# Kernel tuning notes

Measured on AMD Instinct MI355X. Metric: run time of the kernel, lower is better.

Reference implementation:

```python
import jax, jax.numpy as jnp
import numpy as np

B, T1, T2, D, M = 64, 128, 160, 768, 64


def setup_inputs() -> dict:
    key = jax.random.key(0)
    k1, k2, k3 = jax.random.split(key, 3)
    v1 = jax.random.normal(k1, (B, T1, D), dtype=jnp.float32)
    v2 = jax.random.normal(k2, (B, T2, D), dtype=jnp.float32)
    # keras 'uniform' initializer: U(-0.05, 0.05); kernel logical shape (1,1,M,D) -> (M,D)
    kernel = jax.random.uniform(k3, (M, D), dtype=jnp.float32, minval=-0.05, maxval=0.05)
    return {"v1": v1, "v2": v2, "kernel": kernel}


def reference(v1, v2, kernel):
    # Original: expand v1 to [b,t1,1,m,d]*kernel, v2 to [b,1,t2,1,d],
    # numerator = sum_d(v1*v2), cosine_norm=False -> tanh(numerator).
    # Fused as a single einsum contraction over d (avoids [b,t1,t2,m,d] intermediate).
    num = jnp.einsum('bid,md,bjd->bijm', v1, kernel, v2)  # [b,t1,t2,m]
    return jnp.tanh(num)
```

## Files before the change

### kernel.cpp

```cpp
#include <hip/hip_runtime.h>
#include <hip/hip_bf16.h>

namespace {

constexpr int Bn = 64, T1 = 128, T2 = 160, D = 768, M = 64;
constexpr int NTOT = T2 * M;
constexpr int BM = 128;
constexpr int BN = 128;
constexpr int BK = 32;
constexpr int KSTEPS = D / BK;

typedef __bf16 bf16x8 __attribute__((ext_vector_type(8)));
typedef __bf16 bf16x4 __attribute__((ext_vector_type(4)));
typedef float  f32x4  __attribute__((ext_vector_type(4)));

__device__ __forceinline__ float fast_tanh(float x) {
  float e = __expf(2.0f * x);
  return 1.0f - 2.0f * __builtin_amdgcn_rcpf(e + 1.0f);
}

__global__ void cvt_bf16(const float* __restrict__ x, __bf16* __restrict__ y, int n4) {
  int i = blockIdx.x * blockDim.x + threadIdx.x;
  if (i < n4) {
    f32x4 v = ((const f32x4*)x)[i];
    bf16x4 o;
    o[0] = (__bf16)v.x; o[1] = (__bf16)v.y; o[2] = (__bf16)v.z; o[3] = (__bf16)v.w;
    ((bf16x4*)y)[i] = o;
  }
}

__device__ __forceinline__ bf16x8 mul_bb(uint4 a, uint4 b) {
  const unsigned hm = 0xffff0000u;
  bf16x8 r;
  float al, ah, bl, bh;
  al = __uint_as_float(a.x << 16); ah = __uint_as_float(a.x & hm);
  bl = __uint_as_float(b.x << 16); bh = __uint_as_float(b.x & hm);
  r[0] = (__bf16)(al * bl); r[1] = (__bf16)(ah * bh);
  al = __uint_as_float(a.y << 16); ah = __uint_as_float(a.y & hm);
  bl = __uint_as_float(b.y << 16); bh = __uint_as_float(b.y & hm);
  r[2] = (__bf16)(al * bl); r[3] = (__bf16)(ah * bh);
  al = __uint_as_float(a.z << 16); ah = __uint_as_float(a.z & hm);
  bl = __uint_as_float(b.z << 16); bh = __uint_as_float(b.z & hm);
  r[4] = (__bf16)(al * bl); r[5] = (__bf16)(ah * bh);
  al = __uint_as_float(a.w << 16); ah = __uint_as_float(a.w & hm);
  bl = __uint_as_float(b.w << 16); bh = __uint_as_float(b.w & hm);
  r[6] = (__bf16)(al * bl); r[7] = (__bf16)(ah * bh);
  return r;
}

__launch_bounds__(256, 4)
__global__ void mpcos_fast(const __bf16* __restrict__ v1b,
                           const __bf16* __restrict__ v2b,
                           const __bf16* __restrict__ kb,
                           float* __restrict__ out) {
  __shared__ __bf16 Al[2][BM * BK];
  __shared__ __bf16 Bl[2][BN * BK];

  const int t    = threadIdx.x;
  const int lane = t & 63;
  const int w    = t >> 6;
  const int bjm  = blockIdx.x;
  const int bb   = blockIdx.y;

  const int sm = t >> 2, sc = t & 3;
  const __bf16* kp   = kb + sm * D + sc * 8;
  const __bf16* v2p0 = v2b + ((size_t)(bb * T2 + bjm * 2)) * D + sc * 8;
  const __bf16* v2p1 = v2p0 + D;
  const int boff = sm * BK + ((sc ^ ((sm >> 1) & 3)) * 8);

  const int arow = w * 32 + (lane >> 2);
  const int achk = (lane & 3) ^ ((lane >> 3) & 3);
  const __bf16* av1 = v1b + ((size_t)bb * T1 + arow) * D + achk * 8;
  const int adst = (w * 32) * BK;

  const int wrow = (w & 1) * 64;
  const int wcol = (w >> 1) * 64;
  const int lr = lane & 15, lg = lane >> 4;
  const int swc = (lg ^ ((lr >> 1) & 3)) * 8;

  f32x4 acc[4][4] = {};

  {
#pragma unroll
    for (int q = 0; q < 2; ++q)
      __builtin_amdgcn_global_load_lds(
          (const __attribute__((address_space(1))) void*)(av1 + q * 16 * D),
          (__attribute__((address_space(3))) void*)&Al[0][adst + q * 16 * BK],
          16, 0, 0);
    uint4 k0 = *(const uint4*)kp;
    uint4 u0 = *(const uint4*)v2p0;
    uint4 u1 = *(const uint4*)v2p1;
    *(bf16x8*)&Bl[0][boff]            = mul_bb(k0, u0);
    *(bf16x8*)&Bl[0][64 * BK + boff]  = mul_bb(k0, u1);
    __syncthreads();
  }

  int cur = 0;
  for (int ks = 0; ks < KSTEPS; ++ks) {
    const int nxt = cur ^ 1;
    const bool more = (ks + 1 < KSTEPS);
    uint4 pk, pu0, pu1;
    if (more) {
      const int ko = (ks + 1) * BK;
#pragma unroll
      for (int q = 0; q < 2; ++q)
        __builtin_amdgcn_global_load_lds(
            (const __attribute__((address_space(1))) void*)(av1 + ko + q * 16 * D),
            (__attribute__((address_space(3))) void*)&Al[nxt][adst + q * 16 * BK],
            16, 0, 0);
      pk  = *(const uint4*)(kp + ko);
      pu0 = *(const uint4*)(v2p0 + ko);
      pu1 = *(const uint4*)(v2p1 + ko);
    }

    bf16x8 af[4], bfr[4];
#pragma unroll
    for (int ii = 0; ii < 4; ++ii)
      af[ii] = *(const bf16x8*)&Al[cur][(wrow + ii * 16 + lr) * BK + swc];
#pragma unroll
    for (int jj = 0; jj < 4; ++jj)
      bfr[jj] = *(const bf16x8*)&Bl[cur][(wcol + jj * 16 + lr) * BK + swc];
#pragma unroll
    for (int ii = 0; ii < 4; ++ii)
#pragma unroll
      for (int jj = 0; jj < 4; ++jj)
        acc[ii][jj] = __builtin_amdgcn_mfma_f32_16x16x32_bf16(
            af[ii], bfr[jj], acc[ii][jj], 0, 0, 0);

    if (more) {
      *(bf16x8*)&Bl[nxt][boff]           = mul_bb(pk, pu0);
      *(bf16x8*)&Bl[nxt][64 * BK + boff] = mul_bb(pk, pu1);
      __syncthreads();
    }
    cur = nxt;
  }

  float* obase = out + (size_t)bb * T1 * NTOT + (size_t)bjm * BN;
#pragma unroll
  for (int ii = 0; ii < 4; ++ii) {
#pragma unroll
    for (int r = 0; r < 4; ++r) {
      const int row = wrow + ii * 16 + lg * 4 + r;
      float* orow = obase + (size_t)row * NTOT + wcol + lr;
#pragma unroll
      for (int jj = 0; jj < 4; ++jj)
        orow[jj * 16] = fast_tanh(acc[ii][jj][r]);
    }
  }
}

__launch_bounds__(256, 3)
__global__ void mpcos_ref(const float* __restrict__ v1f,
                          const float* __restrict__ v2,
                          const float* __restrict__ kern,
                          float* __restrict__ out) {
  constexpr int BKr = 64;
  __shared__ __bf16 Alds[BM * BKr];
  __shared__ __bf16 Blds[BN * BKr];

  const int t = threadIdx.x, lane = t & 63, w = t >> 6;
  const int bjm = blockIdx.x, bb = blockIdx.y;
  const int srow = t >> 1, sc4 = (t & 1) * 4;
  const int sm = srow & (M - 1), sj = srow >> 6, ssw = srow & 7;
  const float* kp  = kern + sm * D + sc4 * 8;
  const float* v2p = v2 + ((size_t)(bb * T2 + bjm * 2 + sj)) * D + sc4 * 8;
  const float* v1p = v1f + ((size_t)bb * T1 + srow) * D + sc4 * 8;
  const int wrow = (w & 1) * 64, wcol = (w >> 1) * 64;
  const int lr = lane & 15, lg = lane >> 4, lr7 = lr & 7;

  f32x4 acc[4][4] = {};
  for (int ks = 0; ks < D / BKr; ++ks) {
    const int kb = ks * BKr;
    __syncthreads();
    const f32x4* a4 = (const f32x4*)(v1p + kb);
#pragma unroll
    for (int q = 0; q < 4; ++q) {
      f32x4 x0 = a4[2 * q], x1 = a4[2 * q + 1];
      bf16x8 wv;
      wv[0] = (__bf16)x0.x; wv[1] = (__bf16)x0.y; wv[2] = (__bf16)x0.z; wv[3] = (__bf16)x0.w;
      wv[4] = (__bf16)x1.x; wv[5] = (__bf16)x1.y; wv[6] = (__bf16)x1.z; wv[7] = (__bf16)x1.w;
      *(bf16x8*)&Alds[srow * BKr + (((sc4 + q) ^ ssw) * 8)] = wv;
    }
    const f32x4* k4 = (const f32x4*)(kp + kb);
    const f32x4* u4 = (const f32x4*)(v2p + kb);
#pragma unroll
    for (int q = 0; q < 4; ++q) {
      f32x4 a0 = k4[2 * q], a1 = k4[2 * q + 1];
      f32x4 b0 = u4[2 * q], b1 = u4[2 * q + 1];
      bf16x8 wv;
      wv[0] = (__bf16)(a0.x * b0.x); wv[1] = (__bf16)(a0.y * b0.y);
      wv[2] = (__bf16)(a0.z * b0.z); wv[3] = (__bf16)(a0.w * b0.w);
      wv[4] = (__bf16)(a1.x * b1.x); wv[5] = (__bf16)(a1.y * b1.y);
      wv[6] = (__bf16)(a1.z * b1.z); wv[7] = (__bf16)(a1.w * b1.w);
      *(bf16x8*)&Blds[srow * BKr + (((sc4 + q) ^ ssw) * 8)] = wv;
    }
    __syncthreads();
#pragma unroll
    for (int kk = 0; kk < BKr; kk += 32) {
      const int cb = kk >> 3;
      const int st = (((cb + lg) ^ lr7) * 8);
      bf16x8 af[4], bfr[4];
#pragma unroll
      for (int ii = 0; ii < 4; ++ii)
        af[ii] = *(const bf16x8*)&Alds[(wrow + ii * 16 + lr) * BKr + st];
#pragma unroll
      for (int jj = 0; jj < 4; ++jj)
        bfr[jj] = *(const bf16x8*)&Blds[(wcol + jj * 16 + lr) * BKr + st];
#pragma unroll
      for (int ii = 0; ii < 4; ++ii)
#pragma unroll
        for (int jj = 0; jj < 4; ++jj)
          acc[ii][jj] = __builtin_amdgcn_mfma_f32_16x16x32_bf16(
              af[ii], bfr[jj], acc[ii][jj], 0, 0, 0);
    }
  }
  float* obase = out + (size_t)bb * T1 * NTOT + (size_t)bjm * BN;
#pragma unroll
  for (int ii = 0; ii < 4; ++ii)
#pragma unroll
    for (int r = 0; r < 4; ++r) {
      const int row = wrow + ii * 16 + lg * 4 + r;
      float* orow = obase + (size_t)row * NTOT + wcol + lr;
#pragma unroll
      for (int jj = 0; jj < 4; ++jj)
        orow[jj * 16] = fast_tanh(acc[ii][jj][r]);
    }
}

}

extern "C" void kernel_launch(void* const* d_in, const int* in_sizes, int n_in,
                              void* d_out, int out_size, void* d_ws, size_t ws_size,
                              hipStream_t stream) {
  const float* v1   = (const float*)d_in[0];
  const float* v2   = (const float*)d_in[1];
  const float* kern = (const float*)d_in[2];
  float* out = (float*)d_out;

  const size_t n_v1 = (size_t)Bn * T1 * D;
  const size_t n_v2 = (size_t)Bn * T2 * D;
  const size_t n_k  = (size_t)M * D;
  const size_t off_v2 = n_v1 * 2;
  const size_t off_k  = off_v2 + n_v2 * 2;
  const size_t need   = off_k + n_k * 2;

  if (ws_size >= need) {
    __bf16* v1b = (__bf16*)((char*)d_ws);
    __bf16* v2b = (__bf16*)((char*)d_ws + off_v2);
    __bf16* kb  = (__bf16*)((char*)d_ws + off_k);
    cvt_bf16<<<(int)(n_v1 / 4 / 256), 256, 0, stream>>>(v1, v1b, (int)(n_v1 / 4));
    cvt_bf16<<<(int)(n_v2 / 4 / 256), 256, 0, stream>>>(v2, v2b, (int)(n_v2 / 4));
    cvt_bf16<<<(int)(n_k  / 4 / 256), 256, 0, stream>>>(kern, kb, (int)(n_k / 4));
    mpcos_fast<<<dim3(NTOT / BN, Bn), 256, 0, stream>>>(v1b, v2b, kb, out);
  } else {
    mpcos_ref<<<dim3(NTOT / BN, Bn), 256, 0, stream>>>(v1, v2, kern, out);
  }
}
```

Baseline: 495.9 us.

## Deepen GEMM pipeline to prefetch two K-steps ahead with manual waitcnt barriers

Adds a third LDS buffer for the A tile and keeps two K-steps of global loads in flight: A tiles go to LDS via global_load_lds two steps ahead, and kernel/v2 registers are prefetched two steps ahead with ping-pong register sets. The __syncthreads calls are replaced by explicit s_waitcnt vmcnt(5) plus s_barrier, so the newest loads can stay outstanding across the barrier. The main loop is fully unrolled, and the kernel-times-v2 products are computed in one fused helper that converts each kernel component once and reuses it for both v2 rows. This hides more global memory latency behind the MFMA work. In exchange it uses more LDS and registers, and the hand-counted vmcnt value must stay correct.

```diff
diff --git a/kernel.cpp b/kernel.cpp
--- a/kernel.cpp
+++ b/kernel.cpp
@@ -29,23 +29,19 @@
   }
 }
 
-__device__ __forceinline__ bf16x8 mul_bb(uint4 a, uint4 b) {
+__device__ __forceinline__ void mul_bb2(uint4 a, uint4 b0, uint4 b1,
+                                        bf16x8& r0, bf16x8& r1) {
   const unsigned hm = 0xffff0000u;
-  bf16x8 r;
-  float al, ah, bl, bh;
-  al = __uint_as_float(a.x << 16); ah = __uint_as_float(a.x & hm);
-  bl = __uint_as_float(b.x << 16); bh = __uint_as_float(b.x & hm);
-  r[0] = (__bf16)(al * bl); r[1] = (__bf16)(ah * bh);
-  al = __uint_as_float(a.y << 16); ah = __uint_as_float(a.y & hm);
-  bl = __uint_as_float(b.y << 16); bh = __uint_as_float(b.y & hm);
-  r[2] = (__bf16)(al * bl); r[3] = (__bf16)(ah * bh);
-  al = __uint_as_float(a.z << 16); ah = __uint_as_float(a.z & hm);
-  bl = __uint_as_float(b.z << 16); bh = __uint_as_float(b.z & hm);
-  r[4] = (__bf16)(al * bl); r[5] = (__bf16)(ah * bh);
-  al = __uint_as_float(a.w << 16); ah = __uint_as_float(a.w & hm);
-  bl = __uint_as_float(b.w << 16); bh = __uint_as_float(b.w & hm);
-  r[6] = (__bf16)(al * bl); r[7] = (__bf16)(ah * bh);
-  return r;
+#define MPC_COMP(c, i0, i1)                                                   \
+  {                                                                           \
+    float al = __uint_as_float(a.c << 16), ah = __uint_as_float(a.c & hm);    \
+    r0[i0] = (__bf16)(al * __uint_as_float(b0.c << 16));                      \
+    r0[i1] = (__bf16)(ah * __uint_as_float(b0.c & hm));                       \
+    r1[i0] = (__bf16)(al * __uint_as_float(b1.c << 16));                      \
+    r1[i1] = (__bf16)(ah * __uint_as_float(b1.c & hm));                       \
+  }
+  MPC_COMP(x, 0, 1) MPC_COMP(y, 2, 3) MPC_COMP(z, 4, 5) MPC_COMP(w, 6, 7)
+#undef MPC_COMP
 }
 
 __launch_bounds__(256, 4)
@@ -53,7 +49,7 @@
                            const __bf16* __restrict__ v2b,
                            const __bf16* __restrict__ kb,
                            float* __restrict__ out) {
-  __shared__ __bf16 Al[2][BM * BK];
+  __shared__ __bf16 Al[3][BM * BK];
   __shared__ __bf16 Bl[2][BN * BK];
 
   const int t    = threadIdx.x;
@@ -79,61 +75,83 @@
   const int swc = (lg ^ ((lr >> 1) & 3)) * 8;
 
   f32x4 acc[4][4] = {};
-
-  {
+  uint4 pk[2], pu0[2], pu1[2];
+
+  auto stageA = [&](int ks, int buf) {
+    const int ko = ks * BK;
 #pragma unroll
     for (int q = 0; q < 2; ++q)
       __builtin_amdgcn_global_load_lds(
-          (const __attribute__((address_space(1))) void*)(av1 + q * 16 * D),
-          (__attribute__((address_space(3))) void*)&Al[0][adst + q * 16 * BK],
+          (const __attribute__((address_space(1))) void*)(av1 + ko + q * 16 * D),
+          (__attribute__((address_space(3))) void*)&Al[buf][adst + q * 16 * BK],
           16, 0, 0);
+  };
+  auto compute = [&](int abuf, int bbuf) {
+    bf16x8 af[4], bfr[4];
+#pragma unroll
+    for (int ii = 0; ii < 4; ++ii)
+      af[ii] = *(const bf16x8*)&Al[abuf][(wrow + ii * 16 + lr) * BK + swc];
+#pragma unroll
+    for (int jj = 0; jj < 4; ++jj)
+      bfr[jj] = *(const bf16x8*)&Bl[bbuf][(wcol + jj * 16 + lr) * BK + swc];
+#pragma unroll
+    for (int ii = 0; ii < 4; ++ii)
+#pragma unroll
+      for (int jj = 0; jj < 4; ++jj)
+        acc[ii][jj] = __builtin_amdgcn_mfma_f32_16x16x32_bf16(
+            af[ii], bfr[jj], acc[ii][jj], 0, 0, 0);
+  };
+
+  {
     uint4 k0 = *(const uint4*)kp;
     uint4 u0 = *(const uint4*)v2p0;
     uint4 u1 = *(const uint4*)v2p1;
-    *(bf16x8*)&Bl[0][boff]            = mul_bb(k0, u0);
-    *(bf16x8*)&Bl[0][64 * BK + boff]  = mul_bb(k0, u1);
-    __syncthreads();
-  }
-
-  int cur = 0;
-  for (int ks = 0; ks < KSTEPS; ++ks) {
-    const int nxt = cur ^ 1;
-    const bool more = (ks + 1 < KSTEPS);
-    uint4 pk, pu0, pu1;
-    if (more) {
-      const int ko = (ks + 1) * BK;
-#pragma unroll
-      for (int q = 0; q < 2; ++q)
-        __builtin_amdgcn_global_load_lds(
-            (const __attribute__((address_space(1))) void*)(av1 + ko + q * 16 * D),
-            (__attribute__((address_space(3))) void*)&Al[nxt][adst + q * 16 * BK],
-            16, 0, 0);
-      pk  = *(const uint4*)(kp + ko);
-      pu0 = *(const uint4*)(v2p0 + ko);
-      pu1 = *(const uint4*)(v2p1 + ko);
-    }
-
-    bf16x8 af[4], bfr[4];
-#pragma unroll
-    for (int ii = 0; ii < 4; ++ii)
-      af[ii] = *(const bf16x8*)&Al[cur][(wrow + ii * 16 + lr) * BK + swc];
-#pragma unroll
-    for (int jj = 0; jj < 4; ++jj)
-      bfr[jj] = *(const bf16x8*)&Bl[cur][(wcol + jj * 16 + lr) * BK + swc];
-#pragma unroll
-    for (int ii = 0; ii < 4; ++ii)
-#pragma unroll
-      for (int jj = 0; jj < 4; ++jj)
-        acc[ii][jj] = __builtin_amdgcn_mfma_f32_16x16x32_bf16(
-            af[ii], bfr[jj], acc[ii][jj], 0, 0, 0);
-
-    if (more) {
-      *(bf16x8*)&Bl[nxt][boff]           = mul_bb(pk, pu0);
-      *(bf16x8*)&Bl[nxt][64 * BK + boff] = mul_bb(pk, pu1);
-      __syncthreads();
-    }
-    cur = nxt;
-  }
+    stageA(0, 0);
+    stageA(1, 1);
+    pk[1]  = *(const uint4*)(kp + BK);
+    pu0[1] = *(const uint4*)(v2p0 + BK);
+    pu1[1] = *(const uint4*)(v2p1 + BK);
+    bf16x8 r0, r1;
+    mul_bb2(k0, u0, u1, r0, r1);
+    *(bf16x8*)&Bl[0][boff]           = r0;
+    *(bf16x8*)&Bl[0][64 * BK + boff] = r1;
+    asm volatile("s_waitcnt vmcnt(5) lgkmcnt(0)" ::: "memory");
+    __builtin_amdgcn_s_barrier();
+    asm volatile("" ::: "memory");
+  }
+
+#pragma unroll
+  for (int ks = 0; ks < KSTEPS - 2; ++ks) {
+    const int ko2 = (ks + 2) * BK;
+    const int s2 = (ks + 2) & 1, s1 = (ks + 1) & 1;
+    pk[s2]  = *(const uint4*)(kp + ko2);
+    pu0[s2] = *(const uint4*)(v2p0 + ko2);
+    pu1[s2] = *(const uint4*)(v2p1 + ko2);
+    stageA(ks + 2, (ks + 2) % 3);
+
+    compute(ks % 3, ks & 1);
+
+    bf16x8 r0, r1;
+    mul_bb2(pk[s1], pu0[s1], pu1[s1], r0, r1);
+    *(bf16x8*)&Bl[s1][boff]           = r0;
+    *(bf16x8*)&Bl[s1][64 * BK + boff] = r1;
+
+    asm volatile("s_waitcnt vmcnt(5) lgkmcnt(0)" ::: "memory");
+    __builtin_amdgcn_s_barrier();
+    asm volatile("" ::: "memory");
+  }
+
+  {
+    compute((KSTEPS - 2) % 3, (KSTEPS - 2) & 1);
+    bf16x8 r0, r1;
+    mul_bb2(pk[1], pu0[1], pu1[1], r0, r1);
+    *(bf16x8*)&Bl[1][boff]           = r0;
+    *(bf16x8*)&Bl[1][64 * BK + boff] = r1;
+    asm volatile("s_waitcnt vmcnt(0) lgkmcnt(0)" ::: "memory");
+    __builtin_amdgcn_s_barrier();
+    asm volatile("" ::: "memory");
+  }
+  compute((KSTEPS - 1) % 3, (KSTEPS - 1) & 1);
 
   float* obase = out + (size_t)bb * T1 * NTOT + (size_t)bjm * BN;
 #pragma unroll
```

Result: slower. 585.9 us (+18.1%).

## Stage epilogue through LDS for 16-byte coalesced output stores

Applied to the files above, without the earlier changes.

The epilogue now writes tanh results into a padded LDS buffer that reuses the A/B tile memory through a union. Each thread then reads back float4 vectors and issues 128-bit coalesced global stores, replacing the scattered per-element 4-byte stores. The bf16 product helper is also merged so one kernel-vector unpack serves both v2 rows. The staging adds eight block barriers and extra LDS traffic to the epilogue in exchange for wider output writes.

```diff
diff --git a/kernel.cpp b/kernel.cpp
--- a/kernel.cpp
+++ b/kernel.cpp
@@ -29,23 +29,19 @@
   }
 }
 
-__device__ __forceinline__ bf16x8 mul_bb(uint4 a, uint4 b) {
+__device__ __forceinline__ void mul_bb2(uint4 a, uint4 b0, uint4 b1,
+                                        bf16x8& r0, bf16x8& r1) {
   const unsigned hm = 0xffff0000u;
-  bf16x8 r;
-  float al, ah, bl, bh;
-  al = __uint_as_float(a.x << 16); ah = __uint_as_float(a.x & hm);
-  bl = __uint_as_float(b.x << 16); bh = __uint_as_float(b.x & hm);
-  r[0] = (__bf16)(al * bl); r[1] = (__bf16)(ah * bh);
-  al = __uint_as_float(a.y << 16); ah = __uint_as_float(a.y & hm);
-  bl = __uint_as_float(b.y << 16); bh = __uint_as_float(b.y & hm);
-  r[2] = (__bf16)(al * bl); r[3] = (__bf16)(ah * bh);
-  al = __uint_as_float(a.z << 16); ah = __uint_as_float(a.z & hm);
-  bl = __uint_as_float(b.z << 16); bh = __uint_as_float(b.z & hm);
-  r[4] = (__bf16)(al * bl); r[5] = (__bf16)(ah * bh);
-  al = __uint_as_float(a.w << 16); ah = __uint_as_float(a.w & hm);
-  bl = __uint_as_float(b.w << 16); bh = __uint_as_float(b.w & hm);
-  r[6] = (__bf16)(al * bl); r[7] = (__bf16)(ah * bh);
-  return r;
+#define MPC_COMP(c, i0, i1)                                                   \
+  {                                                                           \
+    float al = __uint_as_float(a.c << 16), ah = __uint_as_float(a.c & hm);    \
+    r0[i0] = (__bf16)(al * __uint_as_float(b0.c << 16));                      \
+    r0[i1] = (__bf16)(ah * __uint_as_float(b0.c & hm));                       \
+    r1[i0] = (__bf16)(al * __uint_as_float(b1.c << 16));                      \
+    r1[i1] = (__bf16)(ah * __uint_as_float(b1.c & hm));                       \
+  }
+  MPC_COMP(x, 0, 1) MPC_COMP(y, 2, 3) MPC_COMP(z, 4, 5) MPC_COMP(w, 6, 7)
+#undef MPC_COMP
 }
 
 __launch_bounds__(256, 4)
@@ -53,8 +49,15 @@
                            const __bf16* __restrict__ v2b,
                            const __bf16* __restrict__ kb,
                            float* __restrict__ out) {
-  __shared__ __bf16 Al[2][BM * BK];
-  __shared__ __bf16 Bl[2][BN * BK];
+  struct SmemT {
+    union {
+      struct { __bf16 A[2][BM * BK]; __bf16 B[2][BN * BK]; } g;
+      float c[32 * 132];
+    };
+  };
+  __shared__ SmemT sm;
+  auto& Al = sm.g.A;
+  auto& Bl = sm.g.B;
 
   const int t    = threadIdx.x;
   const int lane = t & 63;
@@ -62,11 +65,11 @@
   const int bjm  = blockIdx.x;
   const int bb   = blockIdx.y;
 
-  const int sm = t >> 2, sc = t & 3;
-  const __bf16* kp   = kb + sm * D + sc * 8;
+  const int sm_ = t >> 2, sc = t & 3;
+  const __bf16* kp   = kb + sm_ * D + sc * 8;
   const __bf16* v2p0 = v2b + ((size_t)(bb * T2 + bjm * 2)) * D + sc * 8;
   const __bf16* v2p1 = v2p0 + D;
-  const int boff = sm * BK + ((sc ^ ((sm >> 1) & 3)) * 8);
+  const int boff = sm_ * BK + ((sc ^ ((sm_ >> 1) & 3)) * 8);
 
   const int arow = w * 32 + (lane >> 2);
   const int achk = (lane & 3) ^ ((lane >> 3) & 3);
@@ -90,8 +93,10 @@
     uint4 k0 = *(const uint4*)kp;
     uint4 u0 = *(const uint4*)v2p0;
     uint4 u1 = *(const uint4*)v2p1;
-    *(bf16x8*)&Bl[0][boff]            = mul_bb(k0, u0);
-    *(bf16x8*)&Bl[0][64 * BK + boff]  = mul_bb(k0, u1);
+    bf16x8 r0, r1;
+    mul_bb2(k0, u0, u1, r0, r1);
+    *(bf16x8*)&Bl[0][boff]           = r0;
+    *(bf16x8*)&Bl[0][64 * BK + boff] = r1;
     __syncthreads();
   }
 
@@ -128,23 +133,35 @@
             af[ii], bfr[jj], acc[ii][jj], 0, 0, 0);
 
     if (more) {
-      *(bf16x8*)&Bl[nxt][boff]           = mul_bb(pk, pu0);
-      *(bf16x8*)&Bl[nxt][64 * BK + boff] = mul_bb(pk, pu1);
+      bf16x8 r0, r1;
+      mul_bb2(pk, pu0, pu1, r0, r1);
+      *(bf16x8*)&Bl[nxt][boff]           = r0;
+      *(bf16x8*)&Bl[nxt][64 * BK + boff] = r1;
       __syncthreads();
     }
     cur = nxt;
   }
 
   float* obase = out + (size_t)bb * T1 * NTOT + (size_t)bjm * BN;
+  const int prow_base = (w & 1) * 16 + lg * 4;
+  const int pcol = wcol + lr;
+  const int rrow = t >> 5;
+  const int rc4  = t & 31;
 #pragma unroll
   for (int ii = 0; ii < 4; ++ii) {
-#pragma unroll
-    for (int r = 0; r < 4; ++r) {
-      const int row = wrow + ii * 16 + lg * 4 + r;
-      float* orow = obase + (size_t)row * NTOT + wcol + lr;
-#pragma unroll
-      for (int jj = 0; jj < 4; ++jj)
-        orow[jj * 16] = fast_tanh(acc[ii][jj][r]);
+    __syncthreads();
+#pragma unroll
+    for (int jj = 0; jj < 4; ++jj)
+#pragma unroll
+      for (int r = 0; r < 4; ++r)
+        sm.c[(prow_base + r) * 132 + pcol + jj * 16] = fast_tanh(acc[ii][jj][r]);
+    __syncthreads();
+#pragma unroll
+    for (int rr = 0; rr < 4; ++rr) {
+      const int pr = rr * 8 + rrow;
+      const int brow = ((pr >> 4) * 64) + ii * 16 + (pr & 15);
+      f32x4 v = *(const f32x4*)&sm.c[pr * 132 + rc4 * 4];
+      *(f32x4*)&obase[(size_t)brow * NTOT + rc4 * 4] = v;
     }
   }
 }
```

New measurement: 639.4 us. +28.9%, slower.

## Build B operand in registers, swap MFMA operands, vectorize stores, remap blocks

Applied to the files above, without the earlier changes.

Removes the shared-memory B tile. Each wave now loads kernel and v2 slices straight into registers and forms the kernel*v2 product per lane, feeding it to the MFMA as the A operand so the transposed accumulator layout allows 16-byte vectorized output stores. Workgroups are also remapped so batches are interleaved across groups of eight. This cuts LDS traffic and store instructions but makes each wave issue more redundant global loads of the kernel, and those loads are no longer prefetched a step ahead.

```diff
diff --git a/kernel.cpp b/kernel.cpp
--- a/kernel.cpp
+++ b/kernel.cpp
@@ -9,6 +9,8 @@
 constexpr int BN = 128;
 constexpr int BK = 32;
 constexpr int KSTEPS = D / BK;
+constexpr int NBJM = NTOT / BN;
+constexpr int NWG  = NBJM * Bn;
 
 typedef __bf16 bf16x8 __attribute__((ext_vector_type(8)));
 typedef __bf16 bf16x4 __attribute__((ext_vector_type(4)));
@@ -54,19 +56,15 @@
                            const __bf16* __restrict__ kb,
                            float* __restrict__ out) {
   __shared__ __bf16 Al[2][BM * BK];
-  __shared__ __bf16 Bl[2][BN * BK];
 
   const int t    = threadIdx.x;
   const int lane = t & 63;
   const int w    = t >> 6;
-  const int bjm  = blockIdx.x;
-  const int bb   = blockIdx.y;
-
-  const int sm = t >> 2, sc = t & 3;
-  const __bf16* kp   = kb + sm * D + sc * 8;
-  const __bf16* v2p0 = v2b + ((size_t)(bb * T2 + bjm * 2)) * D + sc * 8;
-  const __bf16* v2p1 = v2p0 + D;
-  const int boff = sm * BK + ((sc ^ ((sm >> 1) & 3)) * 8);
+
+  const int flat = blockIdx.y * NBJM + blockIdx.x;
+  const int r    = flat >> 3;
+  const int bjm  = r % NBJM;
+  const int bb   = (flat & 7) + 8 * (r / NBJM);
 
   const int arow = w * 32 + (lane >> 2);
   const int achk = (lane & 3) ^ ((lane >> 3) & 3);
@@ -77,6 +75,10 @@
   const int wcol = (w >> 1) * 64;
   const int lr = lane & 15, lg = lane >> 4;
   const int swc = (lg ^ ((lr >> 1) & 3)) * 8;
+
+  const int jrow = wcol >> 6;
+  const __bf16* v2p = v2b + ((size_t)(bb * T2 + bjm * 2 + jrow)) * D + lg * 8;
+  const __bf16* kp  = kb + (size_t)lr * D + lg * 8;
 
   f32x4 acc[4][4] = {};
 
@@ -87,11 +89,6 @@
           (const __attribute__((address_space(1))) void*)(av1 + q * 16 * D),
           (__attribute__((address_space(3))) void*)&Al[0][adst + q * 16 * BK],
           16, 0, 0);
-    uint4 k0 = *(const uint4*)kp;
-    uint4 u0 = *(const uint4*)v2p0;
-    uint4 u1 = *(const uint4*)v2p1;
-    *(bf16x8*)&Bl[0][boff]            = mul_bb(k0, u0);
-    *(bf16x8*)&Bl[0][64 * BK + boff]  = mul_bb(k0, u1);
     __syncthreads();
   }
 
@@ -99,52 +96,64 @@
   for (int ks = 0; ks < KSTEPS; ++ks) {
     const int nxt = cur ^ 1;
     const bool more = (ks + 1 < KSTEPS);
-    uint4 pk, pu0, pu1;
+    const int ko = ks * BK;
+
+    uint4 vv  = *(const uint4*)(v2p + ko);
+    uint4 kv0 = *(const uint4*)(kp + ko);
+    uint4 kv1 = *(const uint4*)(kp + 16 * D + ko);
+    uint4 kv2 = *(const uint4*)(kp + 32 * D + ko);
+    uint4 kv3 = *(const uint4*)(kp + 48 * D + ko);
+
     if (more) {
-      const int ko = (ks + 1) * BK;
+      const int ko1 = ko + BK;
 #pragma unroll
       for (int q = 0; q < 2; ++q)
         __builtin_amdgcn_global_load_lds(
-            (const __attribute__((address_space(1))) void*)(av1 + ko + q * 16 * D),
+            (const __attribute__((address_space(1))) void*)(av1 + ko1 + q * 16 * D),
             (__attribute__((address_space(3))) void*)&Al[nxt][adst + q * 16 * BK],
             16, 0, 0);
-      pk  = *(const uint4*)(kp + ko);
-      pu0 = *(const uint4*)(v2p0 + ko);
-      pu1 = *(const uint4*)(v2p1 + ko);
-    }
-
-    bf16x8 af[4], bfr[4];
+    }
+
+    bf16x8 af[4];
 #pragma unroll
     for (int ii = 0; ii < 4; ++ii)
       af[ii] = *(const bf16x8*)&Al[cur][(wrow + ii * 16 + lr) * BK + swc];
-#pragma unroll
-    for (int jj = 0; jj < 4; ++jj)
-      bfr[jj] = *(const bf16x8*)&Bl[cur][(wcol + jj * 16 + lr) * BK + swc];
-#pragma unroll
-    for (int ii = 0; ii < 4; ++ii)
-#pragma unroll
-      for (int jj = 0; jj < 4; ++jj)
-        acc[ii][jj] = __builtin_amdgcn_mfma_f32_16x16x32_bf16(
-            af[ii], bfr[jj], acc[ii][jj], 0, 0, 0);
-
-    if (more) {
-      *(bf16x8*)&Bl[nxt][boff]           = mul_bb(pk, pu0);
-      *(bf16x8*)&Bl[nxt][64 * BK + boff] = mul_bb(pk, pu1);
-      __syncthreads();
-    }
+
+    {
+      bf16x8 pb;
+      pb = mul_bb(kv0, vv);
+#pragma unroll
+      for (int ii = 0; ii < 4; ++ii)
+        acc[0][ii] = __builtin_amdgcn_mfma_f32_16x16x32_bf16(pb, af[ii], acc[0][ii], 0, 0, 0);
+      pb = mul_bb(kv1, vv);
+#pragma unroll
+      for (int ii = 0; ii < 4; ++ii)
+        acc[1][ii] = __builtin_amdgcn_mfma_f32_16x16x32_bf16(pb, af[ii], acc[1][ii], 0, 0, 0);
+      pb = mul_bb(kv2, vv);
+#pragma unroll
+      for (int ii = 0; ii < 4; ++ii)
+        acc[2][ii] = __builtin_amdgcn_mfma_f32_16x16x32_bf16(pb, af[ii], acc[2][ii], 0, 0, 0);
+      pb = mul_bb(kv3, vv);
+#pragma unroll
+      for (int ii = 0; ii < 4; ++ii)
+        acc[3][ii] = __builtin_amdgcn_mfma_f32_16x16x32_bf16(pb, af[ii], acc[3][ii], 0, 0, 0);
+    }
+
+    if (more) __syncthreads();
     cur = nxt;
   }
 
   float* obase = out + (size_t)bb * T1 * NTOT + (size_t)bjm * BN;
 #pragma unroll
-  for (int ii = 0; ii < 4; ++ii) {
-#pragma unroll
-    for (int r = 0; r < 4; ++r) {
-      const int row = wrow + ii * 16 + lg * 4 + r;
-      float* orow = obase + (size_t)row * NTOT + wcol + lr;
-#pragma unroll
-      for (int jj = 0; jj < 4; ++jj)
-        orow[jj * 16] = fast_tanh(acc[ii][jj][r]);
+  for (int jj = 0; jj < 4; ++jj) {
+#pragma unroll
+    for (int ii = 0; ii < 4; ++ii) {
+      const int row = wrow + ii * 16 + lr;
+      const int col = wcol + jj * 16 + lg * 4;
+      f32x4 v;
+#pragma unroll
+      for (int r2 = 0; r2 < 4; ++r2) v[r2] = fast_tanh(acc[jj][ii][r2]);
+      *(f32x4*)&obase[(size_t)row * NTOT + col] = v;
     }
   }
 }
@@ -154,9 +163,10 @@
                           const float* __restrict__ v2,
                           const float* __restrict__ kern,
                           float* __restrict__ out) {
+  constexpr int BNr = 128;
   constexpr int BKr = 64;
   __shared__ __bf16 Alds[BM * BKr];
-  __shared__ __bf16 Blds[BN * BKr];
+  __shared__ __bf16 Blds[BNr * BKr];
 
   const int t = threadIdx.x, lane = t & 63, w = t >> 6;
   const int bjm = blockIdx.x, bb = blockIdx.y;
@@ -214,7 +224,7 @@
               af[ii], bfr[jj], acc[ii][jj], 0, 0, 0);
     }
   }
-  float* obase = out + (size_t)bb * T1 * NTOT + (size_t)bjm * BN;
+  float* obase = out + (size_t)bb * T1 * NTOT + (size_t)bjm * BNr;
 #pragma unroll
   for (int ii = 0; ii < 4; ++ii)
 #pragma unroll
@@ -251,8 +261,8 @@
     cvt_bf16<<<(int)(n_v1 / 4 / 256), 256, 0, stream>>>(v1, v1b, (int)(n_v1 / 4));
     cvt_bf16<<<(int)(n_v2 / 4 / 256), 256, 0, stream>>>(v2, v2b, (int)(n_v2 / 4));
     cvt_bf16<<<(int)(n_k  / 4 / 256), 256, 0, stream>>>(kern, kb, (int)(n_k / 4));
-    mpcos_fast<<<dim3(NTOT / BN, Bn), 256, 0, stream>>>(v1b, v2b, kb, out);
+    mpcos_fast<<<dim3(NBJM, Bn), 256, 0, stream>>>(v1b, v2b, kb, out);
   } else {
-    mpcos_ref<<<dim3(NTOT / BN, Bn), 256, 0, stream>>>(v1, v2, kern, out);
-  }
-}
+    mpcos_ref<<<dim3(NTOT / 128, Bn), 256, 0, stream>>>(v1, v2, kern, out);
+  }
+}
```

Measured after the change: 692.2 us. +39.6%, slower.
